# Optimization experiments

Hardware: AMD Instinct MI355X
Metric: run time of the kernel (lower is better)

## Reference

```python
import jax, jax.numpy as jnp
import numpy as np

E = 512
H = 8
SL = (16, 16, 16)
B = 4
LEN = np.array([768, 640, 704, 600], dtype=np.int32)


def _starts(lengths):
    cs = jnp.cumsum(lengths)
    starts = jnp.concatenate([jnp.zeros((1,), cs.dtype), cs[:-1]])
    return starts, cs


def _tile_within(data, lengths, buffer):
    # per-token causal window [cur, cur-1, ..., cur-L]; slots before sample start come from buffer
    L = buffer.shape[0]
    N = data.shape[0]
    starts, cs = _starts(lengths)
    g = jnp.arange(N)
    sid = jnp.searchsorted(cs, g, side='right')
    qpos = g - starts[sid]
    src = qpos[:, None] - jnp.arange(L + 1)[None, :]  # [N, L+1]
    from_data = src >= 0
    didx = jnp.clip(starts[sid][:, None] + src, 0, N - 1)
    bidx = jnp.clip(L + src, 0, L - 1)
    return jnp.where(from_data[:, :, None], data[didx], buffer[bidx])


def _mlp(h, w1, b1, w2, b2):
    return jax.nn.gelu(h @ w1 + b1, approximate=False) @ w2 + b2


def _selection(eu, lengths, win):
    # faithful port of the no_grad selection block (B > 1 branch)
    N = eu.shape[0]
    starts, _ = _starts(lengths)
    ends = starts + lengths - 1
    running = jnp.cumsum(eu)
    end_u = running[ends]
    sample_u = jnp.concatenate([end_u[:1], end_u[2:] - end_u[1:-1]])
    running = running - jnp.cumsum(jnp.zeros((N,), eu.dtype).at[starts[1:]].set(sample_u))
    offs = jnp.cumsum(jnp.zeros((N,), eu.dtype).at[starts[1:]].set(lengths[:-1].astype(eu.dtype)))
    idxs = jnp.arange(1, N + 1, dtype=eu.dtype) - offs
    selected = (eu > running / idxs) | (idxs <= win)
    csel = jnp.cumsum(selected.astype(jnp.int32))
    end_counts = csel[ends]
    next_lengths = jnp.concatenate([end_counts[:1], end_counts[1:] - end_counts[:-1]])
    take_map = csel - csel[0]  # unique_consecutive inverse of a 0/1-increment cumsum
    return jnp.nonzero(selected)[0], next_lengths, take_map


def _forward(args, lengths, sels):
    (x, kv_w, kv_b, q_w, q_b, proj_w, proj_b, buf0, buf1, buf2,
     d0_w1, d0_b1, d0_w2, d0_b2, d1_w1, d1_b1, d1_w2, d1_b2,
     u0_w1, u0_b1, u0_w2, u0_b2, u1_w1, u1_b1, u1_w2, u1_b2,
     wq, bq, wk, bk, wv, bv, out_w, out_b) = args
    Ls = [int(v) for v in np.asarray(lengths)]
    x_flat = jnp.concatenate([x[b, :Ls[b]] for b in range(len(Ls))])  # [N0, E]
    kv0 = x_flat @ kv_w + kv_b  # [N0, 2E]
    # scale 0
    tiled0 = _tile_within(kv0, lengths, buf0)  # [N0, SL0, 2E]
    eu0 = jax.nn.elu(_mlp(tiled0.reshape(tiled0.shape[0], -1), u0_w1, u0_b1, u0_w2, u0_b2))[:, 0] + 1.0
    s0 = _selection(jax.lax.stop_gradient(eu0), lengths, SL[0]) if sels is None else sels[0]
    sel0, len1, tm0 = s0
    selt0 = jnp.take(tiled0, sel0, 0)
    r0 = jax.nn.softmax(_mlp(selt0.reshape(selt0.shape[0], -1), d0_w1, d0_b1, d0_w2, d0_b2), -1)
    dat1 = jnp.sum(selt0 * r0[:, :, None], -2)  # [N1, 2E]
    util0 = _tile_within(jnp.take(eu0, sel0, 0)[:, None], len1, jnp.zeros((SL[1] - 1, 1), eu0.dtype))
    # scale 1
    tiled1 = _tile_within(dat1, len1, buf1)  # [N1, SL1, 2E]
    eu1 = jax.nn.elu(_mlp(tiled1.reshape(tiled1.shape[0], -1), u1_w1, u1_b1, u1_w2, u1_b2))[:, 0] + 1.0
    s1 = _selection(jax.lax.stop_gradient(eu1), len1, SL[1]) if sels is None else sels[1]
    sel1, len2, tm1 = s1
    selt1 = jnp.take(tiled1, sel1, 0)
    r1 = jax.nn.softmax(_mlp(selt1.reshape(selt1.shape[0], -1), d1_w1, d1_b1, d1_w2, d1_b2), -1)
    dat2 = jnp.sum(selt1 * r1[:, :, None], -2)  # [N2, 2E]
    util1 = _tile_within(jnp.take(eu1, sel1, 0)[:, None], len2, jnp.zeros((SL[2] - 1, 1), eu1.dtype))
    tiled2 = _tile_within(dat2, len2, buf2)  # [N2, SL2, 2E]
    # per-token multi-scale kv context (reconstructed tail of truncated forward)
    idx1 = tm0
    idx2 = jnp.take(tm1, idx1)
    win1 = jnp.take(tiled1, idx1, 0) * jnp.take(util0, idx1, 0)
    win2 = jnp.take(tiled2, idx2, 0) * jnp.take(util1, idx2, 0)
    kv = jnp.concatenate([tiled0, win1, win2], 1)  # [N0, sum(SL), 2E]
    k = kv[..., :E]
    v = kv[..., E:]
    q = x_flat @ q_w + q_b
    N0 = q.shape[0]
    Skv = kv.shape[1]
    hd = E // H
    qh = (q @ wq + bq).reshape(N0, H, hd)
    kh = (k @ wk + bk).reshape(N0, Skv, H, hd)
    vh = (v @ wv + bv).reshape(N0, Skv, H, hd)
    attn = jax.nn.softmax(jnp.einsum('nhd,nshd->nhs', qh, kh) / float(np.sqrt(hd)), -1)
    ctx = jnp.einsum('nhs,nshd->nhd', attn, vh).reshape(N0, E)
    y = (ctx @ out_w + out_b) @ proj_w + proj_b  # dropout in eval mode == identity
    out = jnp.zeros((len(Ls), max(Ls), E), y.dtype)
    off = 0
    for b, Lb in enumerate(Ls):
        out = out.at[b, :Lb].set(y[off:off + Lb])
        off += Lb
    return out, (s0, s1)


def setup_inputs():
    ks = list(jax.random.split(jax.random.key(0), 64))
    it = iter(ks)

    def nrm(shape, s=0.02):
        return jax.random.normal(next(it), shape, jnp.float32) * s

    def uni(shape):
        return jax.random.uniform(next(it), shape, dtype=jnp.float32)

    F = 2 * E
    inp = {
        'x': jax.random.normal(next(it), (B, int(LEN.max()), E), jnp.float32),
        'lengths': jnp.array(LEN),
        'kv_w': nrm((E, F)), 'kv_b': jnp.zeros((F,), jnp.float32),
        'q_w': nrm((E, E)), 'q_b': jnp.zeros((E,), jnp.float32),
        'proj_w': nrm((E, E)), 'proj_b': jnp.zeros((E,), jnp.float32),
        'buf0': uni((SL[0] - 1, F)), 'buf1': uni((SL[1] - 1, F)), 'buf2': uni((SL[2] - 1, F)),
    }
    for li in (0, 1):
        sl = SL[li]
        din, hid = sl * F, sl * 10
        inp['d%d_w1' % li] = nrm((din, hid)); inp['d%d_b1' % li] = jnp.zeros((hid,), jnp.float32)
        inp['d%d_w2' % li] = nrm((hid, sl)); inp['d%d_b2' % li] = jnp.zeros((sl,), jnp.float32)
        inp['u%d_w1' % li] = nrm((din, hid)); inp['u%d_b1' % li] = jnp.zeros((hid,), jnp.float32)
        inp['u%d_w2' % li] = nrm((hid, 1)); inp['u%d_b2' % li] = jnp.zeros((1,), jnp.float32)
    inp.update({'wq': nrm((E, E)), 'bq': jnp.zeros((E,), jnp.float32),
                'wk': nrm((E, E)), 'bk': jnp.zeros((E,), jnp.float32),
                'wv': nrm((E, E)), 'bv': jnp.zeros((E,), jnp.float32),
                'out_w': nrm((E, E)), 'out_b': jnp.zeros((E,), jnp.float32)})
    return inp


def reference(x, lengths, kv_w, kv_b, q_w, q_b, proj_w, proj_b, buf0, buf1, buf2,
              d0_w1, d0_b1, d0_w2, d0_b2, d1_w1, d1_b1, d1_w2, d1_b2,
              u0_w1, u0_b1, u0_w2, u0_b2, u1_w1, u1_b1, u1_w2, u1_b2,
              wq, bq, wk, bk, wv, bv, out_w, out_b):
    args = (x, kv_w, kv_b, q_w, q_b, proj_w, proj_b, buf0, buf1, buf2,
            d0_w1, d0_b1, d0_w2, d0_b2, d1_w1, d1_b1, d1_w2, d1_b2,
            u0_w1, u0_b1, u0_w2, u0_b2, u1_w1, u1_b1, u1_w2, u1_b2,
            wq, bq, wk, bk, wv, bv, out_w, out_b)
    out, _ = _forward(args, lengths, None)
    return out
```

## Files before the change

### kernel.cpp

```cpp
#include <hip/hip_runtime.h>
#include <cstddef>

#define DEVFN __device__ __forceinline__

constexpr int N0   = 2712;
constexpr int MAXL = 768;
constexpr int NBAT = 4;
constexpr int E    = 512;
constexpr int F    = 1024;
constexpr int HID  = 160;
constexpr int WSZ  = 16;
constexpr int NY   = 2 * WSZ * HID;
constexpr int XSTR = 2560;
constexpr size_t NOFF = (size_t)-1;

constexpr size_t oXF    = 0;
constexpr size_t oXO    = oXF    + (size_t)N0*E;
constexpr size_t oEU0   = oXO    + (size_t)N0*XSTR;
constexpr size_t oDAT1  = oEU0   + (size_t)N0;
constexpr size_t oEU1   = oDAT1  + (size_t)N0*F;
constexpr size_t oDAT2  = oEU1   + (size_t)N0;
constexpr size_t oBH0K  = oDAT2  + (size_t)N0*F;
constexpr size_t oBH0V  = oBH0K  + (size_t)15*E;
constexpr size_t oDH1K  = oBH0V  + (size_t)15*E;
constexpr size_t oDH1V  = oDH1K  + (size_t)N0*E;
constexpr size_t oDH2K  = oDH1V  + (size_t)N0*E;
constexpr size_t oDH2V  = oDH2K  + (size_t)N0*E;
constexpr size_t oCTX   = oDH2V  + (size_t)N0*E;
constexpr size_t oY2    = oCTX   + (size_t)N0*E;
constexpr size_t oEUS0  = oY2    + (size_t)N0*E;
constexpr size_t oEUS1  = oEUS0  + (size_t)N0;
constexpr size_t oSEL0  = oEUS1  + (size_t)N0;
constexpr size_t oTM0   = oSEL0  + (size_t)N0;
constexpr size_t oSEL1  = oTM0   + (size_t)N0;
constexpr size_t oTM1   = oSEL1  + (size_t)N0;
constexpr size_t oB0    = oTM1   + (size_t)N0;
constexpr size_t oB1    = oB0    + 8;
constexpr size_t oB2    = oB1    + 8;
constexpr size_t oWOP   = oB2    + 8;
constexpr size_t oBOP   = oWOP   + (size_t)E*E;
constexpr size_t oWX    = oBOP   + E;
constexpr size_t oXB    = oWX    + (size_t)E*XSTR;
constexpr size_t oBD0   = oXB    + XSTR;
constexpr size_t oBD1   = oBD0   + (size_t)F*NY;
constexpr size_t oBUFY0 = oBD1   + (size_t)F*NY;
constexpr size_t oBUFY1 = oBUFY0 + (size_t)15*NY;
constexpr size_t oYB    = oBUFY1 + (size_t)15*NY;
constexpr size_t oEND   = oYB    + (size_t)N0*NY;

__device__ float g_pool[oEND];

DEVFN float geluf(float x) {
    return 0.5f * x * (1.0f + erff(x / 1.41421356237309504880f));
}

__global__ void k_init() {
    if (threadIdx.x == 0) {
        int* b = (int*)(g_pool + oB0);
        b[0] = 0; b[1] = 768; b[2] = 1408; b[3] = 2112; b[4] = N0;
    }
}

__global__ __launch_bounds__(256) void k_xflat(const float* __restrict__ x) {
    int idx = blockIdx.x * 256 + threadIdx.x;
    if (idx >= N0 * E) return;
    int d = idx & (E - 1);
    int g = idx >> 9;
    int s = (g >= 768) + (g >= 1408) + (g >= 2112);
    const int st[4] = {0, 768, 1408, 2112};
    int qp = g - st[s];
    g_pool[oXF + idx] = x[((size_t)s * MAXL + qp) * E + d];
}

__global__ __launch_bounds__(256) void k_reshape(
    const float* __restrict__ uw, const float* __restrict__ dw, size_t bdOff)
{
    int idx = blockIdx.x * 256 + threadIdx.x;
    if (idx >= F * NY) return;
    int col = idx % NY;
    int f = idx / NY;
    const float* src = (col < NY / 2) ? uw : dw;
    int rem = (col < NY / 2) ? col : col - NY / 2;
    int j = rem / HID, n = rem % HID;
    g_pool[bdOff + idx] = src[((size_t)j * F + f) * HID + n];
}

__global__ __launch_bounds__(256) void k_copymat(
    const float* __restrict__ src, size_t dstOff, int rows, int cols, int lds, int ldd)
{
    int idx = blockIdx.x * 256 + threadIdx.x;
    if (idx >= rows * cols) return;
    int r = idx / cols, c = idx % cols;
    g_pool[dstOff + (size_t)r * ldd + c] = src[(size_t)r * lds + c];
}

__global__ __launch_bounds__(256) void k_prepvec(
    const float* __restrict__ kv_b, const float* __restrict__ q_b, const float* __restrict__ out_b,
    const float* __restrict__ wk, const float* __restrict__ bk,
    const float* __restrict__ wv, const float* __restrict__ bv,
    const float* __restrict__ wq, const float* __restrict__ bq,
    const float* __restrict__ proj_w, const float* __restrict__ proj_b)
{
    int idx = blockIdx.x * 256 + threadIdx.x;
    if (idx >= 3072) return;
    if (idx < 1024) { g_pool[oXB + idx] = kv_b[idx]; return; }
    const float* vec; const float* W; const float* add; int n; size_t dst;
    if (idx < 1536)      { n = idx - 1024; vec = kv_b;     W = wk;     add = bk;     dst = oXB + idx; }
    else if (idx < 2048) { n = idx - 1536; vec = kv_b + E; W = wv;     add = bv;     dst = oXB + idx; }
    else if (idx < 2560) { n = idx - 2048; vec = q_b;      W = wq;     add = bq;     dst = oXB + idx; }
    else                 { n = idx - 2560; vec = out_b;    W = proj_w; add = proj_b; dst = oBOP + n; }
    float s = add[n];
    for (int k = 0; k < E; ++k) s = fmaf(vec[k], W[(size_t)k * E + n], s);
    g_pool[dst] = s;
}

DEVFN void gemm64_body(
    const float* __restrict__ A, int lda,
    const float* __restrict__ B, int ldb,
    const float* __restrict__ bias,
    float* __restrict__ C, int ldc,
    int mval, int row0, int col0, int K, int N)
{
    __shared__ __align__(16) float As[32][68];
    __shared__ __align__(16) float Bs[32][64];

    int tid = threadIdx.x;
    float acc[4][4] = {};
    int tx = tid & 15, ty = tid >> 4;

    for (int k0 = 0; k0 < K; k0 += 32) {
        #pragma unroll
        for (int l = 0; l < 8; ++l) {
            int idx = tid + l * 256;
            int kk = idx & 31, m = idx >> 5;
            int r = row0 + m;
            float v = 0.0f;
            if (r < mval) v = A[(size_t)r * lda + k0 + kk];
            As[kk][m] = v;
        }
        #pragma unroll
        for (int l = 0; l < 8; ++l) {
            int idx = tid + l * 256;
            int n = idx & 63, kk = idx >> 6;
            int col = col0 + n;
            float v = 0.0f;
            if (col < N) v = B[(size_t)(k0 + kk) * ldb + col];
            Bs[kk][n] = v;
        }
        __syncthreads();
        #pragma unroll
        for (int kk = 0; kk < 32; ++kk) {
            float4 a4 = *(const float4*)&As[kk][ty * 4];
            float4 b4 = *(const float4*)&Bs[kk][tx * 4];
            float av[4] = {a4.x, a4.y, a4.z, a4.w};
            float bv[4] = {b4.x, b4.y, b4.z, b4.w};
            #pragma unroll
            for (int i = 0; i < 4; ++i)
                #pragma unroll
                for (int jn = 0; jn < 4; ++jn)
                    acc[i][jn] = fmaf(av[i], bv[jn], acc[i][jn]);
        }
        __syncthreads();
    }

    #pragma unroll
    for (int i = 0; i < 4; ++i) {
        int r = row0 + ty * 4 + i;
        if (r >= mval) continue;
        #pragma unroll
        for (int jn = 0; jn < 4; ++jn) {
            int col = col0 + tx * 4 + jn;
            if (col < N)
                C[(size_t)r * ldc + col] = acc[i][jn] + (bias ? bias[col] : 0.0f);
        }
    }
}

__global__ __launch_bounds__(256) void k_pgemm(
    size_t Aoff, int lda, size_t Boff, int ldb, size_t biasOff,
    size_t Coff, int ldc, int M, size_t mdevOff, int K, int N)
{
    int mval = (mdevOff == NOFF) ? M : *(const int*)(g_pool + mdevOff);
    int row0 = blockIdx.x * 64, col0 = blockIdx.y * 64;
    if (row0 >= mval) return;
    gemm64_body(g_pool + Aoff, lda, g_pool + Boff, ldb,
                (biasOff == NOFF) ? nullptr : g_pool + biasOff,
                g_pool + Coff, ldc, mval, row0, col0, K, N);
}

__global__ __launch_bounds__(256) void k_wprep(
    const float* __restrict__ kv_w, const float* __restrict__ q_w, const float* __restrict__ out_w,
    const float* __restrict__ wk, const float* __restrict__ wv,
    const float* __restrict__ wq, const float* __restrict__ proj_w)
{
    int z = blockIdx.z;
    const float* A; int lda; const float* B; float* C; int ldc;
    if (z == 0)      { A = kv_w;     lda = F; B = wk;     C = g_pool + oWX + 1024; ldc = XSTR; }
    else if (z == 1) { A = kv_w + E; lda = F; B = wv;     C = g_pool + oWX + 1536; ldc = XSTR; }
    else if (z == 2) { A = q_w;      lda = E; B = wq;     C = g_pool + oWX + 2048; ldc = XSTR; }
    else             { A = out_w;    lda = E; B = proj_w; C = g_pool + oWOP;       ldc = E;    }
    gemm64_body(A, lda, B, E, nullptr, C, ldc, E, blockIdx.x * 64, blockIdx.y * 64, E, E);
}

__global__ __launch_bounds__(256) void k_bufy(
    const float* __restrict__ buf0, const float* __restrict__ buf1)
{
    int z = blockIdx.z;
    const float* A = z ? buf1 : buf0;
    const float* B = g_pool + (z ? oBD1 : oBD0);
    float* C = g_pool + (z ? oBUFY1 : oBUFY0);
    gemm64_body(A, F, B, NY, nullptr, C, NY, 15, 0, blockIdx.y * 64, F, NY);
}

__global__ __launch_bounds__(256) void k_bh(
    const float* __restrict__ buf0,
    const float* __restrict__ wk, const float* __restrict__ bk,
    const float* __restrict__ wv, const float* __restrict__ bv)
{
    int z = blockIdx.z;
    const float* A = buf0 + (size_t)z * E;
    const float* B = z ? wv : wk;
    const float* bias = z ? bv : bk;
    float* C = g_pool + (z ? oBH0V : oBH0K);
    gemm64_body(A, F, B, E, bias, C, E, 15, 0, blockIdx.y * 64, E, E);
}

DEVFN void fma_8x8(const float4& a0, const float4& a1, const float4& b0, const float4& b1,
                   float2 (&acc)[8][4])
{
    float av[8] = {a0.x, a0.y, a0.z, a0.w, a1.x, a1.y, a1.z, a1.w};
    float2 bv[4] = {make_float2(b0.x, b0.y), make_float2(b0.z, b0.w),
                    make_float2(b1.x, b1.y), make_float2(b1.z, b1.w)};
    #pragma unroll
    for (int i = 0; i < 8; ++i) {
        #pragma unroll
        for (int q = 0; q < 4; ++q) {
            acc[i][q].x = fmaf(av[i], bv[q].x, acc[i][q].x);
            acc[i][q].y = fmaf(av[i], bv[q].y, acc[i][q].y);
        }
    }
}

DEVFN void gemm128_body(
    const float* __restrict__ A, int lda,
    const float* __restrict__ B, int ldb,
    const float* __restrict__ bias,
    float* __restrict__ C, int ldc,
    int mval, int row0, int col0, int K)
{
    __shared__ __align__(16) float As[16][132];
    __shared__ __align__(16) float Bs[16][132];

    int tid = threadIdx.x;
    int tx = tid & 15, ty = tid >> 4;
    float2 acc[8][4] = {};

    int ar = tid >> 1, akq = (tid & 1) * 8;
    int bk = tid >> 4, bnq = (tid & 15) * 8;

    for (int k0 = 0; k0 < K; k0 += 16) {
        {
            float4 v0 = make_float4(0.f, 0.f, 0.f, 0.f), v1 = v0;
            int rr = row0 + ar;
            if (rr < mval) {
                v0 = *(const float4*)&A[(size_t)rr * lda + k0 + akq];
                v1 = *(const float4*)&A[(size_t)rr * lda + k0 + akq + 4];
            }
            As[akq + 0][ar] = v0.x; As[akq + 1][ar] = v0.y;
            As[akq + 2][ar] = v0.z; As[akq + 3][ar] = v0.w;
            As[akq + 4][ar] = v1.x; As[akq + 5][ar] = v1.y;
            As[akq + 6][ar] = v1.z; As[akq + 7][ar] = v1.w;
        }
        {
            const float* bp = &B[(size_t)(k0 + bk) * ldb + col0 + bnq];
            *(float4*)&Bs[bk][bnq]     = *(const float4*)&bp[0];
            *(float4*)&Bs[bk][bnq + 4] = *(const float4*)&bp[4];
        }
        __syncthreads();

        float4 a0A = *(const float4*)&As[0][ty * 8];
        float4 a1A = *(const float4*)&As[0][ty * 8 + 4];
        float4 b0A = *(const float4*)&Bs[0][tx * 4];
        float4 b1A = *(const float4*)&Bs[0][64 + tx * 4];
        #pragma unroll
        for (int kk = 0; kk < 16; kk += 2) {
            float4 a0B = *(const float4*)&As[kk + 1][ty * 8];
            float4 a1B = *(const float4*)&As[kk + 1][ty * 8 + 4];
            float4 b0B = *(const float4*)&Bs[kk + 1][tx * 4];
            float4 b1B = *(const float4*)&Bs[kk + 1][64 + tx * 4];
            fma_8x8(a0A, a1A, b0A, b1A, acc);
            if (kk + 2 < 16) {
                a0A = *(const float4*)&As[kk + 2][ty * 8];
                a1A = *(const float4*)&As[kk + 2][ty * 8 + 4];
                b0A = *(const float4*)&Bs[kk + 2][tx * 4];
                b1A = *(const float4*)&Bs[kk + 2][64 + tx * 4];
            }
            fma_8x8(a0B, a1B, b0B, b1B, acc);
        }
        __syncthreads();
    }

    #pragma unroll
    for (int i = 0; i < 8; ++i) {
        int r = row0 + ty * 8 + i;
        if (r >= mval) continue;
        float o0[4], o1[4];
        o0[0] = acc[i][0].x; o0[1] = acc[i][0].y; o0[2] = acc[i][1].x; o0[3] = acc[i][1].y;
        o1[0] = acc[i][2].x; o1[1] = acc[i][2].y; o1[2] = acc[i][3].x; o1[3] = acc[i][3].y;
        if (bias) {
            #pragma unroll
            for (int jn = 0; jn < 4; ++jn) {
                o0[jn] += bias[col0 + tx * 4 + jn];
                o1[jn] += bias[col0 + 64 + tx * 4 + jn];
            }
        }
        *(float4*)&C[(size_t)r * ldc + col0 + tx * 4]      = *(float4*)&o0[0];
        *(float4*)&C[(size_t)r * ldc + col0 + 64 + tx * 4] = *(float4*)&o1[0];
    }
}

__global__ __launch_bounds__(256) void k_tgemm(
    size_t Aoff, int lda, size_t Boff, int ldb, size_t biasOff,
    size_t Coff, int ldc, int M, size_t mdevOff, int K)
{
    int mval = (mdevOff == NOFF) ? M : *(const int*)(g_pool + mdevOff);
    int row0 = blockIdx.x * 128, col0 = blockIdx.y * 128;
    if (row0 >= mval) return;
    gemm128_body(g_pool + Aoff, lda, g_pool + Boff, ldb,
                 (biasOff == NOFF) ? nullptr : g_pool + biasOff,
                 g_pool + Coff, ldc, mval, row0, col0, K);
}

__global__ __launch_bounds__(256) void k_zgemm(
    const float* __restrict__ wk, const float* __restrict__ wv)
{
    int z = blockIdx.z;
    int mval = *(const int*)(g_pool + ((z < 2) ? (oB1 + 4) : (oB2 + 4)));
    int row0 = blockIdx.x * 64, col0 = blockIdx.y * 64;
    if (row0 >= mval) return;
    const float* A = g_pool + ((z < 2) ? oDAT1 : oDAT2) + (size_t)(z & 1) * E;
    const float* B = (z & 1) ? wv : wk;
    float* C = g_pool + oDH1K + (size_t)z * N0 * E;
    gemm64_body(A, F, B, E, nullptr, C, E, mval, row0, col0, E, E);
}

__global__ void k_huev(
    size_t boundsOff, size_t bufYOff,
    const float* __restrict__ b1, const float* __restrict__ w2, const float* __restrict__ b2,
    size_t euOff, size_t mdevOff, int M)
{
    int i = blockIdx.x;
    int mval = (mdevOff == NOFF) ? M : *(const int*)(g_pool + mdevOff);
    if (i >= mval) return;
    int n = threadIdx.x;

    __shared__ float t[HID];
    const int* bounds = (const int*)(g_pool + boundsOff);
    int b1i = bounds[1], b2i = bounds[2], b3i = bounds[3];
    int s = (i >= b1i) + (i >= b2i) + (i >= b3i);
    int st = (s == 0) ? 0 : ((s == 1) ? b1i : ((s == 2) ? b2i : b3i));
    int qp = i - st;

    const float* Y = g_pool + oYB;
    const float* bufY = g_pool + bufYOff;

    if (n < HID) {
        float acc = b1[n];
        #pragma unroll
        for (int j = 0; j < WSZ; ++j) {
            int sp = qp - j;
            const float* row = (sp >= 0) ? &Y[(size_t)(i - j) * NY]
                                         : &bufY[(size_t)(15 + sp) * NY];
            acc += row[j * HID + n];
        }
        t[n] = geluf(acc) * w2[n];
    }
    __syncthreads();
    if (n == 0) {
        float v = b2[0];
        for (int k = 0; k < HID; ++k) v += t[k];
        v = (v > 0.0f) ? v : expm1f(v);
        g_pool[euOff + i] = v + 1.0f;
    }
}

__global__ __launch_bounds__(256) void k_select(
    size_t euOff, size_t boundsOff, int win,
    size_t selOff, size_t tmOff, size_t euSelOff, size_t boundsNextOff)
{
    __shared__ __align__(16) float se[N0];
    __shared__ __align__(16) float run[N0];
    __shared__ int sFlag[N0];
    __shared__ int sSum[256];
    __shared__ float sCz[NBAT];
    __shared__ int sEc[NBAT];
    __shared__ int sB[5];

    int tid = threadIdx.x;
    const int* bounds = (const int*)(g_pool + boundsOff);
    if (tid < 5) sB[tid] = bounds[tid];
    __syncthreads();
    int N = sB[4];
    for (int i = tid; i < N; i += 256) se[i] = g_pool[euOff + i];
    __syncthreads();

    if (tid == 0) {
        float r = 0.0f;
        int g = 0;
        for (; g + 8 <= N; g += 8) {
            float4 a = *(const float4*)&se[g];
            float4 b4 = *(const float4*)&se[g + 4];
            r += a.x;  run[g]     = r;
            r += a.y;  run[g + 1] = r;
            r += a.z;  run[g + 2] = r;
            r += a.w;  run[g + 3] = r;
            r += b4.x; run[g + 4] = r;
            r += b4.y; run[g + 5] = r;
            r += b4.z; run[g + 6] = r;
            r += b4.w; run[g + 7] = r;
        }
        for (; g < N; ++g) { r += se[g]; run[g] = r; }
        float e0 = run[sB[1] - 1], e1 = run[sB[2] - 1], e2 = run[sB[3] - 1];
        float su0 = e0;
        float su1 = e2 - e1;
        float su2 = run[sB[4] - 1] - e2;
        sCz[0] = 0.0f;
        sCz[1] = su0;
        sCz[2] = su0 + su1;
        sCz[3] = (su0 + su1) + su2;
    }
    __syncthreads();

    for (int g = tid; g < N; g += 256) {
        int seg = (g >= sB[1]) + (g >= sB[2]) + (g >= sB[3]);
        int st = (seg == 0) ? 0 : sB[seg];
        int qp1 = g - st + 1;
        float r2 = run[g] - sCz[seg];
        bool seld = (se[g] > r2 / (float)qp1) || (qp1 <= win);
        sFlag[g] = seld ? 1 : 0;
    }
    __syncthreads();

    int CH = (N + 255) >> 8;
    int lo = tid * CH, hi = min(lo + CH, N);
    {
        int s = 0;
        for (int g = lo; g < hi; ++g) s += sFlag[g];
        sSum[tid] = s;
    }
    __syncthreads();
    if (tid == 0) {
        int acc = 0;
        for (int t = 0; t < 256; ++t) { int v = sSum[t]; sSum[t] = acc; acc += v; }
    }
    __syncthreads();

    int* sel = (int*)(g_pool + selOff);
    int* tm  = (int*)(g_pool + tmOff);
    float* eus = g_pool + euSelOff;
    int* bn  = (int*)(g_pool + boundsNextOff);

    int csel0 = sFlag[0];
    {
        int csel = sSum[tid];
        for (int g = lo; g < hi; ++g) {
            csel += sFlag[g];
            tm[g] = csel - csel0;
            if (sFlag[g]) { sel[csel - 1] = g; eus[csel - 1] = se[g]; }
            #pragma unroll
            for (int s = 0; s < NBAT; ++s)
                if (g == sB[s + 1] - 1) sEc[s] = csel;
        }
    }
    __syncthreads();
    if (tid == 0) {
        bn[0] = 0; bn[1] = sEc[0]; bn[2] = sEc[1]; bn[3] = sEc[2]; bn[4] = sEc[3];
    }
}

__global__ __launch_bounds__(256) void k_rdat(
    size_t boundsOff, size_t bufYOff,
    const float* __restrict__ b1, const float* __restrict__ w2, const float* __restrict__ b2,
    size_t selOff, size_t mdevOff,
    size_t srcOff, int srcStr, const float* __restrict__ buf,
    size_t datOff)
{
    int i = blockIdx.x;
    if (i >= *(const int*)(g_pool + mdevOff)) return;
    const float* src = g_pool + srcOff;
    const int* bounds = (const int*)(g_pool + boundsOff);
    const int* sel = (const int*)(g_pool + selOff);
    float* dat = g_pool + datOff;

    __shared__ float gh[HID];
    __shared__ float sv[WSZ];
    __shared__ float r[WSZ];
    __shared__ int sG, sQp;

    int tid = threadIdx.x;
    if (tid == 0) {
        int g = sel[i];
        int b1i = bounds[1], b2i = bounds[2], b3i = bounds[3];
        int s = (g >= b1i) + (g >= b2i) + (g >= b3i);
        int st = (s == 0) ? 0 : ((s == 1) ? b1i : ((s == 2) ? b2i : b3i));
        sG = g; sQp = g - st;
    }
    __syncthreads();
    int g = sG, qp = sQp;

    if (tid < HID) {
        const float* Y = g_pool + oYB;
        const float* bufY = g_pool + bufYOff;
        float acc = b1[tid];
        #pragma unroll
        for (int j = 0; j < WSZ; ++j) {
            int sp = qp - j;
            const float* row = (sp >= 0) ? &Y[(size_t)(g - j) * NY]
                                         : &bufY[(size_t)(15 + sp) * NY];
            acc += row[NY / 2 + j * HID + tid];
        }
        gh[tid] = geluf(acc);
    }
    __syncthreads();
    if (tid < WSZ) {
        float acc = 0.0f;
        for (int k = 0; k < HID; ++k) acc += gh[k] * w2[k * WSZ + tid];
        sv[tid] = acc + b2[tid];
    }
    __syncthreads();
    if (tid == 0) {
        float m = sv[0];
        for (int t = 1; t < WSZ; ++t) m = fmaxf(m, sv[t]);
        float sum = 0.0f;
        for (int t = 0; t < WSZ; ++t) { float e = expf(sv[t] - m); r[t] = e; sum += e; }
        for (int t = 0; t < WSZ; ++t) r[t] = r[t] / sum;
    }
    __syncthreads();
    for (int f = tid; f < F; f += 256) {
        float acc = 0.0f;
        for (int j = 0; j < WSZ; ++j) {
            int sp = qp - j;
            float v = (sp >= 0) ? src[(size_t)(g - j) * srcStr + f]
                                : buf[(size_t)(15 + sp) * F + f];
            acc = fmaf(r[j], v, acc);
        }
        dat[(size_t)i * F + f] = acc;
    }
}

__global__ __launch_bounds__(512) void k_attn(
    const float* __restrict__ bk, const float* __restrict__ bv)
{
    int g = blockIdx.x;
    const float* XO   = g_pool + oXO;
    const float* BH0k = g_pool + oBH0K;
    const float* BH0v = g_pool + oBH0V;
    const float* DH1k = g_pool + oDH1K;
    const float* DH1v = g_pool + oDH1V;
    const float* DH2k = g_pool + oDH2K;
    const float* DH2v = g_pool + oDH2V;
    const float* eus0 = g_pool + oEUS0;
    const float* eus1 = g_pool + oEUS1;
    const int* tm0 = (const int*)(g_pool + oTM0);
    const int* tm1 = (const int*)(g_pool + oTM1);
    const int* bounds1 = (const int*)(g_pool + oB1);
    const int* bounds2 = (const int*)(g_pool + oB2);

    __shared__ const float* sK[48];
    __shared__ const float* sV[48];
    __shared__ float sScale[48];
    __shared__ __align__(16) float sQ[E], sBk[E], sBv[E];
    __shared__ float sc[48][8];

    int tid = threadIdx.x;
    sQ[tid]  = XO[(size_t)g * XSTR + 2048 + tid];
    sBk[tid] = bk[tid];
    sBv[tid] = bv[tid];

    if (tid < 48) {
        int s = tid;
        const float *pK = nullptr, *pV = nullptr;
        float scl = 0.0f;
        if (s < 16) {
            int s0 = (g >= 768) + (g >= 1408) + (g >= 2112);
            const int st0[4] = {0, 768, 1408, 2112};
            int sp = (g - st0[s0]) - s;
            if (sp >= 0) { pK = XO + (size_t)(g - s) * XSTR + 1024; pV = XO + (size_t)(g - s) * XSTR + 1536; }
            else         { pK = BH0k + (size_t)(15 + sp) * E; pV = BH0v + (size_t)(15 + sp) * E; }
            scl = 1.0f;
        } else if (s < 32) {
            int j = s - 16;
            int i1 = tm0[g];
            int b1 = bounds1[1], b2 = bounds1[2], b3 = bounds1[3];
            int sg = (i1 >= b1) + (i1 >= b2) + (i1 >= b3);
            int st = (sg == 0) ? 0 : ((sg == 1) ? b1 : ((sg == 2) ? b2 : b3));
            int sp = (i1 - st) - j;
            if (sp >= 0) { pK = DH1k + (size_t)(i1 - j) * E; pV = DH1v + (size_t)(i1 - j) * E; scl = eus0[i1 - j]; }
        } else {
            int j = s - 32;
            int i1 = tm0[g];
            int i2 = tm1[i1];
            int b1 = bounds2[1], b2 = bounds2[2], b3 = bounds2[3];
            int sg = (i2 >= b1) + (i2 >= b2) + (i2 >= b3);
            int st = (sg == 0) ? 0 : ((sg == 1) ? b1 : ((sg == 2) ? b2 : b3));
            int sp = (i2 - st) - j;
            if (sp >= 0) { pK = DH2k + (size_t)(i2 - j) * E; pV = DH2v + (size_t)(i2 - j) * E; scl = eus1[i2 - j]; }
        }
        sK[s] = pK; sV[s] = pV; sScale[s] = scl;
    }
    __syncthreads();

    if (tid < 384) {
        int s = tid >> 3, h = tid & 7;
        const float* bp = sK[s];
        float scl = sScale[s];
        float acc = 0.0f;
        int d0 = h * 64;
        if (s < 16) {
            for (int d = 0; d < 64; d += 4) {
                float4 qv = *(const float4*)&sQ[d0 + d];
                float4 kv4 = *(const float4*)&bp[d0 + d];
                acc += qv.x * kv4.x; acc += qv.y * kv4.y;
                acc += qv.z * kv4.z; acc += qv.w * kv4.w;
            }
        } else if (bp) {
            for (int d = 0; d < 64; d += 4) {
                float4 qv = *(const float4*)&sQ[d0 + d];
                float4 kv4 = *(const float4*)&bp[d0 + d];
                float4 bb = *(const float4*)&sBk[d0 + d];
                acc += qv.x * (bb.x + scl * kv4.x); acc += qv.y * (bb.y + scl * kv4.y);
                acc += qv.z * (bb.z + scl * kv4.z); acc += qv.w * (bb.w + scl * kv4.w);
            }
        } else {
            for (int d = 0; d < 64; d += 4) {
                float4 qv = *(const float4*)&sQ[d0 + d];
                float4 bb = *(const float4*)&sBk[d0 + d];
                acc += qv.x * bb.x; acc += qv.y * bb.y;
                acc += qv.z * bb.z; acc += qv.w * bb.w;
            }
        }
        sc[s][h] = acc * 0.125f;
    }
    __syncthreads();

    if (tid < 8) {
        int h = tid;
        float m = sc[0][h];
        for (int s = 1; s < 48; ++s) m = fmaxf(m, sc[s][h]);
        float sum = 0.0f;
        for (int s = 0; s < 48; ++s) { float e = expf(sc[s][h] - m); sc[s][h] = e; sum += e; }
        for (int s = 0; s < 48; ++s) sc[s][h] = sc[s][h] / sum;
    }
    __syncthreads();

    {
        int d = tid, h = d >> 6;
        float acc = 0.0f;
        for (int s = 0; s < 48; ++s) {
            const float* bp = sV[s];
            float vv;
            if (s < 16) vv = bp[d];
            else        vv = sBv[d] + (bp ? sScale[s] * bp[d] : 0.0f);
            acc = fmaf(sc[s][h], vv, acc);
        }
        g_pool[oCTX + (size_t)g * E + d] = acc;
    }
}

__global__ __launch_bounds__(256) void k_scatter(float* __restrict__ out) {
    int idx = blockIdx.x * 256 + threadIdx.x;
    if (idx >= NBAT * MAXL * E) return;
    int d = idx & (E - 1);
    int rest = idx >> 9;
    int p = rest % MAXL, bb = rest / MAXL;
    const int st[4] = {0, 768, 1408, 2112};
    const int ln[4] = {768, 640, 704, 600};
    out[idx] = (p < ln[bb]) ? g_pool[oY2 + (size_t)(st[bb] + p) * E + d] : 0.0f;
}

extern "C" void kernel_launch(void* const* d_in, const int* in_sizes, int n_in,
                              void* d_out, int out_size, void* d_ws, size_t ws_size,
                              hipStream_t stream)
{
    (void)in_sizes; (void)n_in; (void)d_ws; (void)ws_size; (void)out_size;

    const float* x      = (const float*)d_in[0];
    const float* kv_w   = (const float*)d_in[2];
    const float* kv_b   = (const float*)d_in[3];
    const float* q_w    = (const float*)d_in[4];
    const float* q_b    = (const float*)d_in[5];
    const float* proj_w = (const float*)d_in[6];
    const float* proj_b = (const float*)d_in[7];
    const float* buf0   = (const float*)d_in[8];
    const float* buf1   = (const float*)d_in[9];
    const float* d0_w1  = (const float*)d_in[11];
    const float* d0_b1  = (const float*)d_in[12];
    const float* d0_w2  = (const float*)d_in[13];
    const float* d0_b2  = (const float*)d_in[14];
    const float* u0_w1  = (const float*)d_in[15];
    const float* u0_b1  = (const float*)d_in[16];
    const float* u0_w2  = (const float*)d_in[17];
    const float* u0_b2  = (const float*)d_in[18];
    const float* d1_w1  = (const float*)d_in[19];
    const float* d1_b1  = (const float*)d_in[20];
    const float* d1_w2  = (const float*)d_in[21];
    const float* d1_b2  = (const float*)d_in[22];
    const float* u1_w1  = (const float*)d_in[23];
    const float* u1_b1  = (const float*)d_in[24];
    const float* u1_w2  = (const float*)d_in[25];
    const float* u1_b2  = (const float*)d_in[26];
    const float* wq     = (const float*)d_in[27];
    const float* bq     = (const float*)d_in[28];
    const float* wk     = (const float*)d_in[29];
    const float* bk     = (const float*)d_in[30];
    const float* wv     = (const float*)d_in[31];
    const float* bv     = (const float*)d_in[32];
    const float* out_w  = (const float*)d_in[33];
    const float* out_b  = (const float*)d_in[34];

    auto cdiv = [](int a, int b) { return (a + b - 1) / b; };
    auto GT = [&](int M, int N) { return dim3(cdiv(M, 128), cdiv(N, 128)); };

    k_init<<<1, 64, 0, stream>>>();
    k_xflat<<<cdiv(N0 * E, 256), 256, 0, stream>>>(x);

    k_reshape<<<cdiv(F * NY, 256), 256, 0, stream>>>(u0_w1, d0_w1, oBD0);
    k_reshape<<<cdiv(F * NY, 256), 256, 0, stream>>>(u1_w1, d1_w1, oBD1);
    k_copymat<<<cdiv(E * F, 256), 256, 0, stream>>>(kv_w, oWX, E, F, F, XSTR);
    k_wprep<<<dim3(8, 8, 4), 256, 0, stream>>>(kv_w, q_w, out_w, wk, wv, wq, proj_w);
    k_prepvec<<<cdiv(3072, 256), 256, 0, stream>>>(kv_b, q_b, out_b, wk, bk, wv, bv, wq, bq, proj_w, proj_b);
    k_bufy<<<dim3(1, NY / 64, 2), 256, 0, stream>>>(buf0, buf1);
    k_bh<<<dim3(1, E / 64, 2), 256, 0, stream>>>(buf0, wk, bk, wv, bv);

    k_tgemm<<<GT(N0, XSTR), 256, 0, stream>>>(oXF, E, oWX, XSTR, oXB, oXO, XSTR, N0, NOFF, E);

    k_tgemm<<<GT(N0, NY), 256, 0, stream>>>(oXO, XSTR, oBD0, NY, NOFF, oYB, NY, N0, NOFF, F);
    k_huev<<<N0, 160, 0, stream>>>(oB0, oBUFY0, u0_b1, u0_w2, u0_b2, oEU0, NOFF, N0);
    k_select<<<1, 256, 0, stream>>>(oEU0, oB0, WSZ, oSEL0, oTM0, oEUS0, oB1);
    k_rdat<<<N0, 256, 0, stream>>>(oB0, oBUFY0, d0_b1, d0_w2, d0_b2, oSEL0, oB1 + 4, oXO, XSTR, buf0, oDAT1);

    k_tgemm<<<GT(N0, NY), 256, 0, stream>>>(oDAT1, F, oBD1, NY, NOFF, oYB, NY, N0, oB1 + 4, F);
    k_huev<<<N0, 160, 0, stream>>>(oB1, oBUFY1, u1_b1, u1_w2, u1_b2, oEU1, oB1 + 4, N0);
    k_select<<<1, 256, 0, stream>>>(oEU1, oB1, WSZ, oSEL1, oTM1, oEUS1, oB2);
    k_rdat<<<N0, 256, 0, stream>>>(oB1, oBUFY1, d1_b1, d1_w2, d1_b2, oSEL1, oB2 + 4, oDAT1, F, buf1, oDAT2);

    k_zgemm<<<dim3(cdiv(N0, 64), E / 64, 4), 256, 0, stream>>>(wk, wv);

    k_attn<<<N0, 512, 0, stream>>>(bk, bv);
    k_pgemm<<<dim3(cdiv(N0, 64), E / 64), 256, 0, stream>>>(oCTX, E, oWOP, E, oBOP, oY2, E, N0, NOFF, E, E);
    k_scatter<<<cdiv(NBAT * MAXL * E, 256), 256, 0, stream>>>((float*)d_out);
}
```

Baseline: 1.380 ms.

## Fold scale-0 MLP first layer into kv projection via precomputed weight product

Precomputes kv_w @ BD0 as a split-K GEMM with a reduction, plus the matching bias kv_b @ BD0. The products are appended as extra columns of the fused x projection weight, so the scale-0 hidden pre-activations come out of the first GEMM directly. This removes the separate N0 x F x NY GEMM at scale 0 and replaces it with a wider first GEMM over K=512 instead of K=1024, plus a one-off E x F x NY weight product. The cost is a larger output buffer (stride 7680), extra weight-prep kernels, and different floating-point summation order.

```diff
diff --git a/kernel.cpp b/kernel.cpp
--- a/kernel.cpp
+++ b/kernel.cpp
@@ -11,7 +11,8 @@
 constexpr int HID  = 160;
 constexpr int WSZ  = 16;
 constexpr int NY   = 2 * WSZ * HID;
-constexpr int XSTR = 2560;
+constexpr int XSTR = 7680;
+constexpr int YC0  = 2560;
 constexpr size_t NOFF = (size_t)-1;
 
 constexpr size_t oXF    = 0;
@@ -114,6 +115,15 @@
     g_pool[dst] = s;
 }
 
+__global__ __launch_bounds__(256) void k_cvec(const float* __restrict__ kv_b) {
+    int n = blockIdx.x * 256 + threadIdx.x;
+    if (n >= NY) return;
+    const float* BD = g_pool + oBD0;
+    float s = 0.0f;
+    for (int k = 0; k < F; ++k) s = fmaf(kv_b[k], BD[(size_t)k * NY + n], s);
+    g_pool[oXB + YC0 + n] = s;
+}
+
 DEVFN void gemm64_body(
     const float* __restrict__ A, int lda,
     const float* __restrict__ B, int ldb,
@@ -331,6 +341,23 @@
                  g_pool + Coff, ldc, mval, row0, col0, K);
 }
 
+__global__ __launch_bounds__(256) void k_wy(const float* __restrict__ kv_w) {
+    int z = blockIdx.z;
+    const float* A = kv_w + z * 256;
+    const float* B = g_pool + oBD0 + (size_t)z * 256 * NY;
+    float* C = g_pool + oYB + (size_t)z * E * NY;
+    gemm128_body(A, F, B, NY, nullptr, C, NY, E, blockIdx.x * 128, blockIdx.y * 128, 256);
+}
+
+__global__ __launch_bounds__(256) void k_wyred() {
+    int idx = blockIdx.x * 256 + threadIdx.x;
+    if (idx >= E * NY) return;
+    int r = idx / NY, c = idx % NY;
+    const float* p = g_pool + oYB;
+    float s = ((p[idx] + p[(size_t)E * NY + idx]) + p[(size_t)2 * E * NY + idx]) + p[(size_t)3 * E * NY + idx];
+    g_pool[oWX + (size_t)r * XSTR + YC0 + c] = s;
+}
+
 __global__ __launch_bounds__(256) void k_zgemm(
     const float* __restrict__ wk, const float* __restrict__ wv)
 {
@@ -345,7 +372,7 @@
 }
 
 __global__ void k_huev(
-    size_t boundsOff, size_t bufYOff,
+    size_t boundsOff, size_t yOff, int yStr, size_t bufYOff,
     const float* __restrict__ b1, const float* __restrict__ w2, const float* __restrict__ b2,
     size_t euOff, size_t mdevOff, int M)
 {
@@ -361,7 +388,7 @@
     int st = (s == 0) ? 0 : ((s == 1) ? b1i : ((s == 2) ? b2i : b3i));
     int qp = i - st;
 
-    const float* Y = g_pool + oYB;
+    const float* Y = g_pool + yOff;
     const float* bufY = g_pool + bufYOff;
 
     if (n < HID) {
@@ -369,7 +396,7 @@
         #pragma unroll
         for (int j = 0; j < WSZ; ++j) {
             int sp = qp - j;
-            const float* row = (sp >= 0) ? &Y[(size_t)(i - j) * NY]
+            const float* row = (sp >= 0) ? &Y[(size_t)(i - j) * yStr]
                                          : &bufY[(size_t)(15 + sp) * NY];
             acc += row[j * HID + n];
         }
@@ -479,7 +506,7 @@
 }
 
 __global__ __launch_bounds__(256) void k_rdat(
-    size_t boundsOff, size_t bufYOff,
+    size_t boundsOff, size_t yOff, int yStr, size_t bufYOff,
     const float* __restrict__ b1, const float* __restrict__ w2, const float* __restrict__ b2,
     size_t selOff, size_t mdevOff,
     size_t srcOff, int srcStr, const float* __restrict__ buf,
@@ -509,13 +536,13 @@
     int g = sG, qp = sQp;
 
     if (tid < HID) {
-        const float* Y = g_pool + oYB;
+        const float* Y = g_pool + yOff;
         const float* bufY = g_pool + bufYOff;
         float acc = b1[tid];
         #pragma unroll
         for (int j = 0; j < WSZ; ++j) {
             int sp = qp - j;
-            const float* row = (sp >= 0) ? &Y[(size_t)(g - j) * NY]
+            const float* row = (sp >= 0) ? &Y[(size_t)(g - j) * yStr]
                                          : &bufY[(size_t)(15 + sp) * NY];
             acc += row[NY / 2 + j * HID + tid];
         }
@@ -729,20 +756,22 @@
     k_copymat<<<cdiv(E * F, 256), 256, 0, stream>>>(kv_w, oWX, E, F, F, XSTR);
     k_wprep<<<dim3(8, 8, 4), 256, 0, stream>>>(kv_w, q_w, out_w, wk, wv, wq, proj_w);
     k_prepvec<<<cdiv(3072, 256), 256, 0, stream>>>(kv_b, q_b, out_b, wk, bk, wv, bv, wq, bq, proj_w, proj_b);
+    k_cvec<<<cdiv(NY, 256), 256, 0, stream>>>(kv_b);
+    k_wy<<<dim3(4, 40, 4), 256, 0, stream>>>(kv_w);
+    k_wyred<<<cdiv(E * NY, 256), 256, 0, stream>>>();
     k_bufy<<<dim3(1, NY / 64, 2), 256, 0, stream>>>(buf0, buf1);
     k_bh<<<dim3(1, E / 64, 2), 256, 0, stream>>>(buf0, wk, bk, wv, bv);
 
     k_tgemm<<<GT(N0, XSTR), 256, 0, stream>>>(oXF, E, oWX, XSTR, oXB, oXO, XSTR, N0, NOFF, E);
 
-    k_tgemm<<<GT(N0, NY), 256, 0, stream>>>(oXO, XSTR, oBD0, NY, NOFF, oYB, NY, N0, NOFF, F);
-    k_huev<<<N0, 160, 0, stream>>>(oB0, oBUFY0, u0_b1, u0_w2, u0_b2, oEU0, NOFF, N0);
+    k_huev<<<N0, 160, 0, stream>>>(oB0, oXO + YC0, XSTR, oBUFY0, u0_b1, u0_w2, u0_b2, oEU0, NOFF, N0);
     k_select<<<1, 256, 0, stream>>>(oEU0, oB0, WSZ, oSEL0, oTM0, oEUS0, oB1);
-    k_rdat<<<N0, 256, 0, stream>>>(oB0, oBUFY0, d0_b1, d0_w2, d0_b2, oSEL0, oB1 + 4, oXO, XSTR, buf0, oDAT1);
+    k_rdat<<<N0, 256, 0, stream>>>(oB0, oXO + YC0, XSTR, oBUFY0, d0_b1, d0_w2, d0_b2, oSEL0, oB1 + 4, oXO, XSTR, buf0, oDAT1);
 
     k_tgemm<<<GT(N0, NY), 256, 0, stream>>>(oDAT1, F, oBD1, NY, NOFF, oYB, NY, N0, oB1 + 4, F);
-    k_huev<<<N0, 160, 0, stream>>>(oB1, oBUFY1, u1_b1, u1_w2, u1_b2, oEU1, oB1 + 4, N0);
+    k_huev<<<N0, 160, 0, stream>>>(oB1, oYB, NY, oBUFY1, u1_b1, u1_w2, u1_b2, oEU1, oB1 + 4, N0);
     k_select<<<1, 256, 0, stream>>>(oEU1, oB1, WSZ, oSEL1, oTM1, oEUS1, oB2);
-    k_rdat<<<N0, 256, 0, stream>>>(oB1, oBUFY1, d1_b1, d1_w2, d1_b2, oSEL1, oB2 + 4, oDAT1, F, buf1, oDAT2);
+    k_rdat<<<N0, 256, 0, stream>>>(oB1, oYB, NY, oBUFY1, d1_b1, d1_w2, d1_b2, oSEL1, oB2 + 4, oDAT1, F, buf1, oDAT2);
 
     k_zgemm<<<dim3(cdiv(N0, 64), E / 64, 4), 256, 0, stream>>>(wk, wv);
 
```

Result: no change. 1.380 ms (+0.0%).
